# Optimization experiments

Measured on AMD Instinct MI355X. Metric: run time of the kernel, lower is better.

The kernel has to match this reference:

```python
import jax, jax.numpy as jnp
import numpy as np

N = 10000      # nodes
E = 320000     # edges (before self loops)
IN = 128       # in_channels
HID = 128      # hidden_channels
OUT = 64       # out_channels
H = 3          # heads
K = 10         # n_clusters
EDIM = 1       # edge_attr feature dim
NEG_SLOPE = 0.2


def setup_inputs() -> dict:
    key = jax.random.key(0)
    ks = jax.random.split(key, 24)
    x = jax.random.normal(ks[0], (N, IN), jnp.float32)
    src = jax.random.randint(ks[1], (E,), 0, N)
    dst = jax.random.randint(ks[2], (E,), 0, N)
    dst = jnp.where(src == dst, (dst + 1) % N, dst)  # avoid pre-existing self loops
    edge_index = jnp.stack([src, dst]).astype(jnp.int64)
    edge_attr = jax.random.uniform(ks[3], (E, EDIM), dtype=jnp.float32)
    s = 0.1
    inp = {
        'x': x, 'edge_index': edge_index, 'edge_attr': edge_attr,
        # GAT layer 1 params
        'W1': jax.random.normal(ks[4], (IN, H * HID), jnp.float32) * s,
        'att_s1': jax.random.normal(ks[5], (H, HID), jnp.float32) * s,
        'att_d1': jax.random.normal(ks[6], (H, HID), jnp.float32) * s,
        'We1': jax.random.normal(ks[7], (EDIM, H * HID), jnp.float32) * s,
        'att_e1': jax.random.normal(ks[8], (H, HID), jnp.float32) * s,
        'b1': jnp.zeros((H * HID,), jnp.float32),
        # GAT layer 2 params
        'W2': jax.random.normal(ks[9], (H * HID, H * OUT), jnp.float32) * s,
        'att_s2': jax.random.normal(ks[10], (H, OUT), jnp.float32) * s,
        'att_d2': jax.random.normal(ks[11], (H, OUT), jnp.float32) * s,
        'We2': jax.random.normal(ks[12], (EDIM, H * OUT), jnp.float32) * s,
        'att_e2': jax.random.normal(ks[13], (H, OUT), jnp.float32) * s,
        'b2': jnp.zeros((H * OUT,), jnp.float32),
        # cluster head
        'Wp': jax.random.normal(ks[14], (H * OUT, K), jnp.float32) * s,
        'bp': jnp.zeros((K,), jnp.float32),
    }
    return inp


def gat_layer(x, src, dst, eattr, W, att_s, att_d, We, att_e, b, heads, ch):
    n = x.shape[0]
    h = (x @ W).reshape(n, heads, ch)                       # [N,H,C]
    a_s = jnp.einsum('nhc,hc->nh', h, att_s)                # [N,H]
    a_d = jnp.einsum('nhc,hc->nh', h, att_d)
    e = (eattr @ We).reshape(-1, heads, ch)                 # [E,H,C]
    a_e = jnp.einsum('ehc,hc->eh', e, att_e)                # [E,H]
    alpha = jax.nn.leaky_relu(a_s[src] + a_d[dst] + a_e, NEG_SLOPE)
    # segment softmax over destination nodes
    m = jax.ops.segment_max(alpha, dst, num_segments=n)
    ex = jnp.exp(alpha - m[dst])
    denom = jax.ops.segment_sum(ex, dst, num_segments=n)
    coef = ex / (denom[dst] + 1e-16)                        # [E,H]
    msg = h[src] * coef[:, :, None]                         # [E,H,C]
    out = jax.ops.segment_sum(msg, dst, num_segments=n)     # [N,H,C]
    return out.reshape(n, heads * ch) + b


def reference(x, edge_index, edge_attr, W1, att_s1, att_d1, We1, att_e1, b1,
              W2, att_s2, att_d2, We2, att_e2, b2, Wp, bp):
    n = x.shape[0]
    loop = jnp.arange(n, dtype=edge_index.dtype)
    src = jnp.concatenate([edge_index[0], loop])            # add self loops
    dst = jnp.concatenate([edge_index[1], loop])
    ea = jnp.concatenate([edge_attr, jnp.ones((n, edge_attr.shape[1]), edge_attr.dtype)])  # fill_value=1
    h = jnp.nan_to_num(x, nan=0.0)
    h = jax.nn.elu(gat_layer(h, src, dst, ea, W1, att_s1, att_d1, We1, att_e1, b1, H, HID))
    h = gat_layer(h, src, dst, ea, W2, att_s2, att_d2, We2, att_e2, b2, H, OUT)
    z = h / jnp.maximum(jnp.linalg.norm(h, axis=1, keepdims=True), 1e-12)  # F.normalize p=2 dim=1
    A_hat = z @ z.T                                          # [N,N]
    p = jax.nn.softmax(z @ Wp + bp, axis=1)                  # F.softmax picks dim=1 for 2D
    return (A_hat, p, z)
```

## Files before the change

### kernel.cpp

```cpp
#include <hip/hip_runtime.h>
#include <hip/hip_bf16.h>
#include <math.h>

#define NN 10000
#define EE 320000
#define ETOT (EE + NN)
#define INC 128
#define HIDC 128
#define OUTC 64
#define NH 3
#define KCL 10
#define SLOPE 0.2f
#define NPAD 10112

typedef __attribute__((ext_vector_type(8))) short bf16x8;
typedef __attribute__((ext_vector_type(4))) float f32x4;

__device__ __forceinline__ float wave_sum(float v) {
  for (int off = 32; off; off >>= 1) v += __shfl_xor(v, off, 64);
  return v;
}

__device__ __forceinline__ short f2bf(float v) {
  unsigned int u = __float_as_uint(v);
  unsigned int r = (u + 0x7fffu + ((u >> 16) & 1u)) >> 16;
  return (short)r;
}
__device__ __forceinline__ float bf2f(short s) {
  return __uint_as_float(((unsigned int)(unsigned short)s) << 16);
}

__global__ __launch_bounds__(256) void csr_count(const int* __restrict__ dst,
                                                 int* __restrict__ counts,
                                                 int* __restrict__ epos,
                                                 const float* __restrict__ We1,
                                                 const float* __restrict__ ae1,
                                                 const float* __restrict__ We2,
                                                 const float* __restrict__ ae2,
                                                 float* __restrict__ ce) {
  if (blockIdx.x == gridDim.x - 1) {
    int lane = threadIdx.x;
    if (lane < 64) {
      for (int h = 0; h < NH; h++) {
        float p = 0.f;
        for (int c = lane; c < HIDC; c += 64) p += We1[h * HIDC + c] * ae1[h * HIDC + c];
        p = wave_sum(p);
        if (lane == 0) ce[h] = p;
        float q = 0.f;
        for (int c = lane; c < OUTC; c += 64) q += We2[h * OUTC + c] * ae2[h * OUTC + c];
        q = wave_sum(q);
        if (lane == 0) ce[NH + h] = q;
      }
    }
    return;
  }
  int e = blockIdx.x * 256 + threadIdx.x;
  if (e >= ETOT) return;
  int d = (e < EE) ? dst[e] : (e - EE);
  epos[e] = atomicAdd(&counts[d], 1);
}

__global__ __launch_bounds__(1024) void scan_kernel(const int* __restrict__ counts,
                                                    int* __restrict__ offsets) {
  __shared__ int sums[1024];
  const int PT = 10;
  int tid = threadIdx.x;
  int base = tid * PT;
  int loc[PT];
  int run = 0;
#pragma unroll
  for (int j = 0; j < PT; j++) {
    int i = base + j;
    int v = (i < NN) ? counts[i] : 0;
    run += v;
    loc[j] = run;
  }
  sums[tid] = run;
  __syncthreads();
  for (int off = 1; off < 1024; off <<= 1) {
    int t = (tid >= off) ? sums[tid - off] : 0;
    __syncthreads();
    sums[tid] += t;
    __syncthreads();
  }
  int excl = sums[tid] - run;
#pragma unroll
  for (int j = 0; j < PT; j++) {
    int i = base + j;
    if (i < NN) offsets[i + 1] = excl + loc[j];
  }
  if (tid == 0) offsets[0] = 0;
}

__global__ __launch_bounds__(256) void csr_fill(const int* __restrict__ dst,
                                                const int* __restrict__ offsets,
                                                const int* __restrict__ epos,
                                                int* __restrict__ edge_ids) {
  int e = blockIdx.x * 256 + threadIdx.x;
  if (e >= ETOT) return;
  int d = (e < EE) ? dst[e] : (e - EE);
  edge_ids[offsets[d] + epos[e]] = e;
}

template <bool NANFIX>
__global__ __launch_bounds__(256) void gemm_nn_mfma(const float* __restrict__ A,
                                                    const float* __restrict__ B,
                                                    float* __restrict__ C,
                                                    const float* __restrict__ att_s,
                                                    const float* __restrict__ att_d,
                                                    float* __restrict__ as_out,
                                                    float* __restrict__ ad_out,
                                                    int M, int K, int Nc, int ch) {
  __shared__ short Ah[64 * 32], Al[64 * 32];
  __shared__ short Bh[64 * 32], Bl[64 * 32];
  int tid = threadIdx.x;
  int lane = tid & 63, wave = tid >> 6;
  int wm = (wave >> 1) * 32, wn = (wave & 1) * 32;
  int bm = blockIdx.y * 64, bn = blockIdx.x * 64;
  int fr = lane & 15, fk = (lane >> 4) * 8;
  f32x4 acc[2][2] = {};
  int ar = tid >> 2, ac = (tid & 3) * 8;
  int bc = tid & 63, bk0 = tid >> 6;

  for (int k0 = 0; k0 < K; k0 += 32) {
    float av[8];
    if (bm + ar < M) {
      const float* src = A + (size_t)(bm + ar) * K + k0 + ac;
      float4 v0 = *(const float4*)src;
      float4 v1 = *(const float4*)(src + 4);
      av[0] = v0.x; av[1] = v0.y; av[2] = v0.z; av[3] = v0.w;
      av[4] = v1.x; av[5] = v1.y; av[6] = v1.z; av[7] = v1.w;
    } else {
#pragma unroll
      for (int j = 0; j < 8; j++) av[j] = 0.f;
    }
#pragma unroll
    for (int j = 0; j < 8; j++) {
      float v = av[j];
      if (NANFIX) v = (v == v) ? v : 0.f;
      short hs = f2bf(v);
      Ah[ar * 32 + ac + j] = hs;
      Al[ar * 32 + ac + j] = f2bf(v - bf2f(hs));
    }
#pragma unroll
    for (int it = 0; it < 8; it++) {
      int kk = bk0 + it * 4;
      float v = B[(size_t)(k0 + kk) * Nc + bn + bc];
      short hs = f2bf(v);
      Bh[bc * 32 + kk] = hs;
      Bl[bc * 32 + kk] = f2bf(v - bf2f(hs));
    }
    __syncthreads();

    bf16x8 ah[2], al2[2], bh[2], bl2[2];
#pragma unroll
    for (int t = 0; t < 2; t++) {
      ah[t]  = *(const bf16x8*)&Ah[(wm + t * 16 + fr) * 32 + fk];
      al2[t] = *(const bf16x8*)&Al[(wm + t * 16 + fr) * 32 + fk];
      bh[t]  = *(const bf16x8*)&Bh[(wn + t * 16 + fr) * 32 + fk];
      bl2[t] = *(const bf16x8*)&Bl[(wn + t * 16 + fr) * 32 + fk];
    }
#pragma unroll
    for (int i = 0; i < 2; i++)
#pragma unroll
      for (int j = 0; j < 2; j++) {
        acc[i][j] = __builtin_amdgcn_mfma_f32_16x16x32_bf16(ah[i], bh[j], acc[i][j], 0, 0, 0);
        acc[i][j] = __builtin_amdgcn_mfma_f32_16x16x32_bf16(ah[i], bl2[j], acc[i][j], 0, 0, 0);
        acc[i][j] = __builtin_amdgcn_mfma_f32_16x16x32_bf16(al2[i], bh[j], acc[i][j], 0, 0, 0);
      }
    __syncthreads();
  }

  int col0 = lane & 15, rq = (lane >> 4) * 4;
#pragma unroll
  for (int i = 0; i < 2; i++)
#pragma unroll
    for (int v = 0; v < 4; v++) {
      int r = bm + wm + i * 16 + rq + v;
      if (r < M) {
#pragma unroll
        for (int j = 0; j < 2; j++)
          C[(size_t)r * Nc + bn + wn + j * 16 + col0] = acc[i][j][v];
      }
    }

  int head = bn / ch;
  float sax[4], sdx[4];
#pragma unroll
  for (int j = 0; j < 4; j++) {
    int cidx = bn + wn + j * 16 + col0;
    sax[j] = att_s[cidx];
    sdx[j] = att_d[cidx];
  }
#pragma unroll
  for (int i = 0; i < 2; i++)
#pragma unroll
    for (int v = 0; v < 4; v++) {
      float ps = 0.f, pd = 0.f;
#pragma unroll
      for (int j = 0; j < 2; j++) {
        ps += acc[i][j][v] * sax[j];
        pd += acc[i][j][v] * sdx[j];
      }
#pragma unroll
      for (int j = 2; j < 4; j++) {
        ps += acc[i][j & 1][v] * 0.f;
      }
      (void)pd;
      ps = acc[i][0][v] * sax[0] + acc[i][1][v] * sax[1];
      pd = acc[i][0][v] * sdx[0] + acc[i][1][v] * sdx[1];
#pragma unroll
      for (int m = 1; m < 16; m <<= 1) {
        ps += __shfl_xor(ps, m, 64);
        pd += __shfl_xor(pd, m, 64);
      }
      int r = bm + wm + i * 16 + rq + v;
      if ((lane & 15) == 0 && r < M) {
        atomicAdd(&as_out[r * NH + head], ps);
        atomicAdd(&ad_out[r * NH + head], pd);
      }
    }
}

template <int C, bool ELU>
__global__ __launch_bounds__(256) void gat_agg(const float* __restrict__ hfeat,
                                               const float* __restrict__ a_s,
                                               const float* __restrict__ a_d,
                                               const float* __restrict__ ce,
                                               const int* __restrict__ esrc,
                                               const float* __restrict__ ea,
                                               const int* __restrict__ offsets,
                                               const int* __restrict__ edge_ids,
                                               const float* __restrict__ bias,
                                               float* __restrict__ out) {
  const int HC = NH * C;
  int wave = threadIdx.x >> 6, lane = threadIdx.x & 63;
  int n = blockIdx.x * 4 + wave;
  int beg = offsets[n], end = offsets[n + 1];
  float adn0 = a_d[n * NH + 0], adn1 = a_d[n * NH + 1], adn2 = a_d[n * NH + 2];
  float ce0 = ce[0], ce1v = ce[1], ce2 = ce[2];

  float s0 = 0.f, s1 = 0.f, s2 = 0.f;
  float4 a0 = {0.f, 0.f, 0.f, 0.f}, a1 = {0.f, 0.f, 0.f, 0.f};

  for (int base = beg; base < end; base += 64) {
    int i = base + lane;
    int se = 0;
    float e0 = 0.f, e1 = 0.f, e2 = 0.f;
    if (i < end) {
      int e = edge_ids[i];
      float a;
      if (e < EE) { se = esrc[e]; a = ea[e]; } else { se = e - EE; a = 1.f; }
      const float* asr = a_s + NH * se;
      float t0 = asr[0] + adn0 + a * ce0; t0 = t0 > 0.f ? t0 : SLOPE * t0;
      float t1 = asr[1] + adn1 + a * ce1v; t1 = t1 > 0.f ? t1 : SLOPE * t1;
      float t2 = asr[2] + adn2 + a * ce2; t2 = t2 > 0.f ? t2 : SLOPE * t2;
      e0 = __expf(t0); e1 = __expf(t1); e2 = __expf(t2);
      s0 += e0; s1 += e1; s2 += e2;
    }
    int cnt = min(64, end - base);
    for (int t = 0; t < cnt; t++) {
      int s = __shfl(se, t, 64);
      float cc0 = __shfl(e0, t, 64);
      float cc1 = __shfl(e1, t, 64);
      float cc2 = __shfl(e2, t, 64);
      const float4* hr4 = (const float4*)(hfeat + (size_t)s * HC);
      if constexpr (C == 128) {
        float4 v0 = hr4[lane];
        float cA = (lane < 32) ? cc0 : cc1;
        a0.x += v0.x * cA; a0.y += v0.y * cA; a0.z += v0.z * cA; a0.w += v0.w * cA;
        if (lane < 32) {
          float4 v1 = hr4[64 + lane];
          a1.x += v1.x * cc2; a1.y += v1.y * cc2; a1.z += v1.z * cc2; a1.w += v1.w * cc2;
        }
      } else {
        if (lane < 48) {
          float4 v0 = hr4[lane];
          int hd = lane >> 4;
          float cA = (hd == 0) ? cc0 : (hd == 1 ? cc1 : cc2);
          a0.x += v0.x * cA; a0.y += v0.y * cA; a0.z += v0.z * cA; a0.w += v0.w * cA;
        }
      }
    }
  }

  s0 = wave_sum(s0); s1 = wave_sum(s1); s2 = wave_sum(s2);
  float di0 = 1.f / (s0 + 1e-16f), di1 = 1.f / (s1 + 1e-16f), di2 = 1.f / (s2 + 1e-16f);

  if constexpr (C == 128) {
    float dA = (lane < 32) ? di0 : di1;
    float4 b0 = *(const float4*)&bias[4 * lane];
    float x0 = a0.x * dA + b0.x, x1 = a0.y * dA + b0.y;
    float x2 = a0.z * dA + b0.z, x3 = a0.w * dA + b0.w;
    if (ELU) {
      x0 = x0 > 0.f ? x0 : expm1f(x0);
      x1 = x1 > 0.f ? x1 : expm1f(x1);
      x2 = x2 > 0.f ? x2 : expm1f(x2);
      x3 = x3 > 0.f ? x3 : expm1f(x3);
    }
    *(float4*)&out[(size_t)n * HC + 4 * lane] = make_float4(x0, x1, x2, x3);
    if (lane < 32) {
      float4 b1 = *(const float4*)&bias[256 + 4 * lane];
      float y0 = a1.x * di2 + b1.x, y1 = a1.y * di2 + b1.y;
      float y2 = a1.z * di2 + b1.z, y3 = a1.w * di2 + b1.w;
      if (ELU) {
        y0 = y0 > 0.f ? y0 : expm1f(y0);
        y1 = y1 > 0.f ? y1 : expm1f(y1);
        y2 = y2 > 0.f ? y2 : expm1f(y2);
        y3 = y3 > 0.f ? y3 : expm1f(y3);
      }
      *(float4*)&out[(size_t)n * HC + 256 + 4 * lane] = make_float4(y0, y1, y2, y3);
    }
  } else {
    if (lane < 48) {
      int hd = lane >> 4;
      float dA = (hd == 0) ? di0 : (hd == 1 ? di1 : di2);
      float4 b0 = *(const float4*)&bias[4 * lane];
      float x0 = a0.x * dA + b0.x, x1 = a0.y * dA + b0.y;
      float x2 = a0.z * dA + b0.z, x3 = a0.w * dA + b0.w;
      if (ELU) {
        x0 = x0 > 0.f ? x0 : expm1f(x0);
        x1 = x1 > 0.f ? x1 : expm1f(x1);
        x2 = x2 > 0.f ? x2 : expm1f(x2);
        x3 = x3 > 0.f ? x3 : expm1f(x3);
      }
      *(float4*)&out[(size_t)n * HC + 4 * lane] = make_float4(x0, x1, x2, x3);
    }
  }
}

__global__ __launch_bounds__(256) void norm_phead(const float* __restrict__ h2,
                                                  float* __restrict__ z,
                                                  __hip_bfloat16* __restrict__ zb,
                                                  const float* __restrict__ Wp,
                                                  const float* __restrict__ bp,
                                                  float* __restrict__ p) {
  int wave = threadIdx.x >> 6, lane = threadIdx.x & 63;
  int n = blockIdx.x * 4 + wave;
  const float* r = h2 + (size_t)n * 192;
  float v0 = r[lane], v1 = r[lane + 64], v2 = r[lane + 128];
  float s = wave_sum(v0 * v0 + v1 * v1 + v2 * v2);
  float inv = 1.f / fmaxf(sqrtf(s), 1e-12f);
  v0 *= inv; v1 *= inv; v2 *= inv;
  float* zr = z + (size_t)n * 192;
  zr[lane] = v0;
  zr[lane + 64] = v1;
  zr[lane + 128] = v2;
  __hip_bfloat16* zbr = zb + (size_t)n * 192;
  zbr[lane] = __float2bfloat16(v0);
  zbr[lane + 64] = __float2bfloat16(v1);
  zbr[lane + 128] = __float2bfloat16(v2);

  float lg[KCL];
#pragma unroll
  for (int j = 0; j < KCL; j++) {
    float t = v0 * Wp[lane * KCL + j] + v1 * Wp[(lane + 64) * KCL + j] +
              v2 * Wp[(lane + 128) * KCL + j];
    lg[j] = wave_sum(t) + bp[j];
  }
  if (lane == 0) {
    float m = -1e30f;
#pragma unroll
    for (int j = 0; j < KCL; j++) m = fmaxf(m, lg[j]);
    float ex[KCL];
    float sum = 0.f;
#pragma unroll
    for (int j = 0; j < KCL; j++) { ex[j] = expf(lg[j] - m); sum += ex[j]; }
    float invs = 1.f / sum;
#pragma unroll
    for (int j = 0; j < KCL; j++) p[(size_t)n * KCL + j] = ex[j] * invs;
  }
}

__global__ __launch_bounds__(256) void gemm_zzT_mfma(const short* __restrict__ Zb,
                                                     float* __restrict__ C, int N) {
  __shared__ short As[128 * 32];
  __shared__ short Bs[128 * 32];
  int tid = threadIdx.x;
  int lane = tid & 63;
  int wave = tid >> 6;
  int wm = (wave >> 1) * 64, wn = (wave & 1) * 64;
  int bm = blockIdx.y * 128, bn = blockIdx.x * 128;

  f32x4 acc[4][4] = {};

  int lrow = tid >> 2;
  int lcol = (tid & 3) * 8;

  int fr = lane & 15;
  int fk = (lane >> 4) * 8;

  for (int kt = 0; kt < 6; kt++) {
    int k0 = kt * 32;
    const short* ga0 = Zb + (size_t)(bm + lrow) * 192 + k0 + lcol;
    const short* ga1 = Zb + (size_t)(bm + 64 + lrow) * 192 + k0 + lcol;
    const short* gb0 = Zb + (size_t)(bn + lrow) * 192 + k0 + lcol;
    const short* gb1 = Zb + (size_t)(bn + 64 + lrow) * 192 + k0 + lcol;
    __builtin_amdgcn_global_load_lds(
        (const __attribute__((address_space(1))) unsigned int*)ga0,
        (__attribute__((address_space(3))) unsigned int*)&As[lrow * 32 + lcol], 16, 0, 0);
    __builtin_amdgcn_global_load_lds(
        (const __attribute__((address_space(1))) unsigned int*)ga1,
        (__attribute__((address_space(3))) unsigned int*)&As[(64 + lrow) * 32 + lcol], 16, 0, 0);
    __builtin_amdgcn_global_load_lds(
        (const __attribute__((address_space(1))) unsigned int*)gb0,
        (__attribute__((address_space(3))) unsigned int*)&Bs[lrow * 32 + lcol], 16, 0, 0);
    __builtin_amdgcn_global_load_lds(
        (const __attribute__((address_space(1))) unsigned int*)gb1,
        (__attribute__((address_space(3))) unsigned int*)&Bs[(64 + lrow) * 32 + lcol], 16, 0, 0);
    __syncthreads();

    bf16x8 af[4], bfr[4];
#pragma unroll
    for (int t = 0; t < 4; t++) af[t] = *(const bf16x8*)&As[(wm + t * 16 + fr) * 32 + fk];
#pragma unroll
    for (int t = 0; t < 4; t++) bfr[t] = *(const bf16x8*)&Bs[(wn + t * 16 + fr) * 32 + fk];
#pragma unroll
    for (int i = 0; i < 4; i++)
#pragma unroll
      for (int j = 0; j < 4; j++)
        acc[i][j] = __builtin_amdgcn_mfma_f32_16x16x32_bf16(af[i], bfr[j], acc[i][j], 0, 0, 0);
    __syncthreads();
  }

  int col0 = lane & 15;
  int rquad = (lane >> 4) * 4;
#pragma unroll
  for (int i = 0; i < 4; i++) {
#pragma unroll
    for (int v = 0; v < 4; v++) {
      int r = bm + wm + i * 16 + rquad + v;
      if (r >= N) continue;
      size_t ro = (size_t)r * N;
#pragma unroll
      for (int j = 0; j < 4; j++) {
        int c = bn + wn + j * 16 + col0;
        if (c < N) __builtin_nontemporal_store(acc[i][j][v], &C[ro + c]);
      }
    }
  }
}

extern "C" void kernel_launch(void* const* d_in, const int* in_sizes, int n_in,
                              void* d_out, int out_size, void* d_ws, size_t ws_size,
                              hipStream_t stream) {
  const float* x = (const float*)d_in[0];
  const int* edge_index = (const int*)d_in[1];
  const float* edge_attr = (const float*)d_in[2];
  const float* W1 = (const float*)d_in[3];
  const float* att_s1 = (const float*)d_in[4];
  const float* att_d1 = (const float*)d_in[5];
  const float* We1 = (const float*)d_in[6];
  const float* att_e1 = (const float*)d_in[7];
  const float* b1 = (const float*)d_in[8];
  const float* W2 = (const float*)d_in[9];
  const float* att_s2 = (const float*)d_in[10];
  const float* att_d2 = (const float*)d_in[11];
  const float* We2 = (const float*)d_in[12];
  const float* att_e2 = (const float*)d_in[13];
  const float* b2 = (const float*)d_in[14];
  const float* Wp = (const float*)d_in[15];
  const float* bp = (const float*)d_in[16];

  const int* esrc = edge_index;
  const int* edst = edge_index + EE;

  float* A_hat = (float*)d_out;
  float* p_out = A_hat + (size_t)NN * NN;
  float* z_out = p_out + (size_t)NN * KCL;

  char* ws = (char*)d_ws;
  float* h1 = (float*)ws;            ws += sizeof(float) * (size_t)NN * 384;
  float* h1act = (float*)ws;         ws += sizeof(float) * (size_t)NN * 384;
  int* counts = (int*)ws;            ws += sizeof(int) * NN;
  float* as1 = (float*)ws;           ws += sizeof(float) * NN * NH;
  float* ad1 = (float*)ws;           ws += sizeof(float) * NN * NH;
  float* as2 = (float*)ws;           ws += sizeof(float) * NN * NH;
  float* ad2 = (float*)ws;           ws += sizeof(float) * NN * NH;
  float* ce = (float*)ws;            ws += sizeof(float) * 8;
  int* offsets = (int*)ws;           ws += sizeof(int) * (NN + 1);
  int* epos = (int*)ws;              ws += sizeof(int) * ETOT;
  int* edge_ids = (int*)ws;          ws += sizeof(int) * ETOT;
  __hip_bfloat16* zb = (__hip_bfloat16*)ws; ws += sizeof(__hip_bfloat16) * (size_t)NPAD * 192;

  float* h2 = h1;
  float* h2out = h1 + (size_t)NN * 192;

  hipMemsetAsync(counts, 0, sizeof(int) * NN + sizeof(float) * 4 * NN * NH, stream);

  int egrid = (ETOT + 255) / 256;
  csr_count<<<egrid + 1, 256, 0, stream>>>(edst, counts, epos, We1, att_e1, We2, att_e2, ce);
  scan_kernel<<<1, 1024, 0, stream>>>(counts, offsets);
  csr_fill<<<egrid, 256, 0, stream>>>(edst, offsets, epos, edge_ids);

  gemm_nn_mfma<true><<<dim3(384 / 64, (NN + 63) / 64), 256, 0, stream>>>(
      x, W1, h1, att_s1, att_d1, as1, ad1, NN, INC, 384, HIDC);
  gat_agg<HIDC, true><<<NN / 4, 256, 0, stream>>>(h1, as1, ad1, ce, esrc, edge_attr,
                                                  offsets, edge_ids, b1, h1act);

  gemm_nn_mfma<false><<<dim3(192 / 64, (NN + 63) / 64), 256, 0, stream>>>(
      h1act, W2, h2, att_s2, att_d2, as2, ad2, NN, 384, 192, OUTC);
  gat_agg<OUTC, false><<<NN / 4, 256, 0, stream>>>(h2, as2, ad2, ce + NH, esrc, edge_attr,
                                                   offsets, edge_ids, b2, h2out);

  norm_phead<<<NN / 4, 256, 0, stream>>>(h2out, z_out, zb, Wp, bp, p_out);

  gemm_zzT_mfma<<<dim3((NN + 127) / 128, (NN + 127) / 128), 256, 0, stream>>>(
      (const short*)zb, A_hat, NN);
}
```

Before: 686.5 us.

## Pack edge records in CSR, fuse layer-2 aggregation with normalize/head, use 32x32 MFMA

The CSR fill now stores a packed (src, edge_attr) record per sorted edge, so aggregation no longer makes an indirect lookup through edge ids into the source and attribute arrays. The generic aggregation kernel is split into layer-specific versions: layer 1 gets a simpler all-lanes float2 layout, and layer 2 is fused with L2 normalization and the cluster softmax head, which removes one kernel launch and a round-trip of h2out. The zzT GEMM switches from 16x16x32 to 32x32x16 bf16 MFMA tiles, changing fragment loads and the store pattern. In exchange the edge record array doubles in size, and the new store order in the big A_hat write may reduce coalescing.

```diff
diff --git a/kernel.cpp b/kernel.cpp
--- a/kernel.cpp
+++ b/kernel.cpp
@@ -15,6 +15,7 @@
 
 typedef __attribute__((ext_vector_type(8))) short bf16x8;
 typedef __attribute__((ext_vector_type(4))) float f32x4;
+typedef __attribute__((ext_vector_type(16))) float f32x16;
 
 __device__ __forceinline__ float wave_sum(float v) {
   for (int off = 32; off; off >>= 1) v += __shfl_xor(v, off, 64);
@@ -93,13 +94,21 @@
 }
 
 __global__ __launch_bounds__(256) void csr_fill(const int* __restrict__ dst,
+                                                const int* __restrict__ src,
+                                                const float* __restrict__ ea,
                                                 const int* __restrict__ offsets,
                                                 const int* __restrict__ epos,
-                                                int* __restrict__ edge_ids) {
+                                                int2* __restrict__ erec) {
   int e = blockIdx.x * 256 + threadIdx.x;
   if (e >= ETOT) return;
-  int d = (e < EE) ? dst[e] : (e - EE);
-  edge_ids[offsets[d] + epos[e]] = e;
+  int d, s;
+  float a;
+  if (e < EE) {
+    d = dst[e]; s = src[e]; a = ea[e];
+  } else {
+    d = e - EE; s = e - EE; a = 1.f;
+  }
+  erec[offsets[d] + epos[e]] = make_int2(s, __float_as_int(a));
 }
 
 template <bool NANFIX>
@@ -185,30 +194,14 @@
     }
 
   int head = bn / ch;
-  float sax[4], sdx[4];
-#pragma unroll
-  for (int j = 0; j < 4; j++) {
-    int cidx = bn + wn + j * 16 + col0;
-    sax[j] = att_s[cidx];
-    sdx[j] = att_d[cidx];
-  }
+  float sax0 = att_s[bn + wn + col0], sax1 = att_s[bn + wn + 16 + col0];
+  float sdx0 = att_d[bn + wn + col0], sdx1 = att_d[bn + wn + 16 + col0];
 #pragma unroll
   for (int i = 0; i < 2; i++)
 #pragma unroll
     for (int v = 0; v < 4; v++) {
-      float ps = 0.f, pd = 0.f;
-#pragma unroll
-      for (int j = 0; j < 2; j++) {
-        ps += acc[i][j][v] * sax[j];
-        pd += acc[i][j][v] * sdx[j];
-      }
-#pragma unroll
-      for (int j = 2; j < 4; j++) {
-        ps += acc[i][j & 1][v] * 0.f;
-      }
-      (void)pd;
-      ps = acc[i][0][v] * sax[0] + acc[i][1][v] * sax[1];
-      pd = acc[i][0][v] * sdx[0] + acc[i][1][v] * sdx[1];
+      float ps = acc[i][0][v] * sax0 + acc[i][1][v] * sax1;
+      float pd = acc[i][0][v] * sdx0 + acc[i][1][v] * sdx1;
 #pragma unroll
       for (int m = 1; m < 16; m <<= 1) {
         ps += __shfl_xor(ps, m, 64);
@@ -222,18 +215,14 @@
     }
 }
 
-template <int C, bool ELU>
-__global__ __launch_bounds__(256) void gat_agg(const float* __restrict__ hfeat,
-                                               const float* __restrict__ a_s,
-                                               const float* __restrict__ a_d,
-                                               const float* __restrict__ ce,
-                                               const int* __restrict__ esrc,
-                                               const float* __restrict__ ea,
-                                               const int* __restrict__ offsets,
-                                               const int* __restrict__ edge_ids,
-                                               const float* __restrict__ bias,
-                                               float* __restrict__ out) {
-  const int HC = NH * C;
+__global__ __launch_bounds__(256) void gat_agg_l1(const float* __restrict__ hfeat,
+                                                  const float* __restrict__ a_s,
+                                                  const float* __restrict__ a_d,
+                                                  const float* __restrict__ ce,
+                                                  const int* __restrict__ offsets,
+                                                  const int2* __restrict__ erec,
+                                                  const float* __restrict__ bias,
+                                                  float* __restrict__ out) {
   int wave = threadIdx.x >> 6, lane = threadIdx.x & 63;
   int n = blockIdx.x * 4 + wave;
   int beg = offsets[n], end = offsets[n + 1];
@@ -241,16 +230,16 @@
   float ce0 = ce[0], ce1v = ce[1], ce2 = ce[2];
 
   float s0 = 0.f, s1 = 0.f, s2 = 0.f;
-  float4 a0 = {0.f, 0.f, 0.f, 0.f}, a1 = {0.f, 0.f, 0.f, 0.f};
+  float a00 = 0.f, a01 = 0.f, a10 = 0.f, a11 = 0.f, a20 = 0.f, a21 = 0.f;
 
   for (int base = beg; base < end; base += 64) {
     int i = base + lane;
     int se = 0;
     float e0 = 0.f, e1 = 0.f, e2 = 0.f;
     if (i < end) {
-      int e = edge_ids[i];
-      float a;
-      if (e < EE) { se = esrc[e]; a = ea[e]; } else { se = e - EE; a = 1.f; }
+      int2 rec = erec[i];
+      se = rec.x;
+      float a = __int_as_float(rec.y);
       const float* asr = a_s + NH * se;
       float t0 = asr[0] + adn0 + a * ce0; t0 = t0 > 0.f ? t0 : SLOPE * t0;
       float t1 = asr[1] + adn1 + a * ce1v; t1 = t1 > 0.f ? t1 : SLOPE * t1;
@@ -259,77 +248,45 @@
       s0 += e0; s1 += e1; s2 += e2;
     }
     int cnt = min(64, end - base);
+#pragma unroll 2
     for (int t = 0; t < cnt; t++) {
       int s = __shfl(se, t, 64);
-      float cc0 = __shfl(e0, t, 64);
-      float cc1 = __shfl(e1, t, 64);
-      float cc2 = __shfl(e2, t, 64);
-      const float4* hr4 = (const float4*)(hfeat + (size_t)s * HC);
-      if constexpr (C == 128) {
-        float4 v0 = hr4[lane];
-        float cA = (lane < 32) ? cc0 : cc1;
-        a0.x += v0.x * cA; a0.y += v0.y * cA; a0.z += v0.z * cA; a0.w += v0.w * cA;
-        if (lane < 32) {
-          float4 v1 = hr4[64 + lane];
-          a1.x += v1.x * cc2; a1.y += v1.y * cc2; a1.z += v1.z * cc2; a1.w += v1.w * cc2;
-        }
-      } else {
-        if (lane < 48) {
-          float4 v0 = hr4[lane];
-          int hd = lane >> 4;
-          float cA = (hd == 0) ? cc0 : (hd == 1 ? cc1 : cc2);
-          a0.x += v0.x * cA; a0.y += v0.y * cA; a0.z += v0.z * cA; a0.w += v0.w * cA;
-        }
-      }
+      float c0 = __shfl(e0, t, 64);
+      float c1 = __shfl(e1, t, 64);
+      float c2 = __shfl(e2, t, 64);
+      const float2* hr2 = (const float2*)(hfeat + (size_t)s * 384);
+      float2 v0 = hr2[lane], v1 = hr2[lane + 64], v2 = hr2[lane + 128];
+      a00 += v0.x * c0; a01 += v0.y * c0;
+      a10 += v1.x * c1; a11 += v1.y * c1;
+      a20 += v2.x * c2; a21 += v2.y * c2;
     }
   }
 
   s0 = wave_sum(s0); s1 = wave_sum(s1); s2 = wave_sum(s2);
   float di0 = 1.f / (s0 + 1e-16f), di1 = 1.f / (s1 + 1e-16f), di2 = 1.f / (s2 + 1e-16f);
 
-  if constexpr (C == 128) {
-    float dA = (lane < 32) ? di0 : di1;
-    float4 b0 = *(const float4*)&bias[4 * lane];
-    float x0 = a0.x * dA + b0.x, x1 = a0.y * dA + b0.y;
-    float x2 = a0.z * dA + b0.z, x3 = a0.w * dA + b0.w;
-    if (ELU) {
-      x0 = x0 > 0.f ? x0 : expm1f(x0);
-      x1 = x1 > 0.f ? x1 : expm1f(x1);
-      x2 = x2 > 0.f ? x2 : expm1f(x2);
-      x3 = x3 > 0.f ? x3 : expm1f(x3);
-    }
-    *(float4*)&out[(size_t)n * HC + 4 * lane] = make_float4(x0, x1, x2, x3);
-    if (lane < 32) {
-      float4 b1 = *(const float4*)&bias[256 + 4 * lane];
-      float y0 = a1.x * di2 + b1.x, y1 = a1.y * di2 + b1.y;
-      float y2 = a1.z * di2 + b1.z, y3 = a1.w * di2 + b1.w;
-      if (ELU) {
-        y0 = y0 > 0.f ? y0 : expm1f(y0);
-        y1 = y1 > 0.f ? y1 : expm1f(y1);
-        y2 = y2 > 0.f ? y2 : expm1f(y2);
-        y3 = y3 > 0.f ? y3 : expm1f(y3);
-      }
-      *(float4*)&out[(size_t)n * HC + 256 + 4 * lane] = make_float4(y0, y1, y2, y3);
-    }
-  } else {
-    if (lane < 48) {
-      int hd = lane >> 4;
-      float dA = (hd == 0) ? di0 : (hd == 1 ? di1 : di2);
-      float4 b0 = *(const float4*)&bias[4 * lane];
-      float x0 = a0.x * dA + b0.x, x1 = a0.y * dA + b0.y;
-      float x2 = a0.z * dA + b0.z, x3 = a0.w * dA + b0.w;
-      if (ELU) {
-        x0 = x0 > 0.f ? x0 : expm1f(x0);
-        x1 = x1 > 0.f ? x1 : expm1f(x1);
-        x2 = x2 > 0.f ? x2 : expm1f(x2);
-        x3 = x3 > 0.f ? x3 : expm1f(x3);
-      }
-      *(float4*)&out[(size_t)n * HC + 4 * lane] = make_float4(x0, x1, x2, x3);
-    }
-  }
-}
-
-__global__ __launch_bounds__(256) void norm_phead(const float* __restrict__ h2,
+  float2 b0 = *(const float2*)&bias[2 * lane];
+  float2 b1 = *(const float2*)&bias[128 + 2 * lane];
+  float2 b2 = *(const float2*)&bias[256 + 2 * lane];
+  float x0 = a00 * di0 + b0.x, x1 = a01 * di0 + b0.y;
+  float y0 = a10 * di1 + b1.x, y1 = a11 * di1 + b1.y;
+  float z0 = a20 * di2 + b2.x, z1 = a21 * di2 + b2.y;
+  x0 = x0 > 0.f ? x0 : expm1f(x0); x1 = x1 > 0.f ? x1 : expm1f(x1);
+  y0 = y0 > 0.f ? y0 : expm1f(y0); y1 = y1 > 0.f ? y1 : expm1f(y1);
+  z0 = z0 > 0.f ? z0 : expm1f(z0); z1 = z1 > 0.f ? z1 : expm1f(z1);
+  float* orow = out + (size_t)n * 384;
+  *(float2*)&orow[2 * lane] = make_float2(x0, x1);
+  *(float2*)&orow[128 + 2 * lane] = make_float2(y0, y1);
+  *(float2*)&orow[256 + 2 * lane] = make_float2(z0, z1);
+}
+
+__global__ __launch_bounds__(256) void gat_agg_l2(const float* __restrict__ hfeat,
+                                                  const float* __restrict__ a_s,
+                                                  const float* __restrict__ a_d,
+                                                  const float* __restrict__ ce,
+                                                  const int* __restrict__ offsets,
+                                                  const int2* __restrict__ erec,
+                                                  const float* __restrict__ bias,
                                                   float* __restrict__ z,
                                                   __hip_bfloat16* __restrict__ zb,
                                                   const float* __restrict__ Wp,
@@ -337,25 +294,63 @@
                                                   float* __restrict__ p) {
   int wave = threadIdx.x >> 6, lane = threadIdx.x & 63;
   int n = blockIdx.x * 4 + wave;
-  const float* r = h2 + (size_t)n * 192;
-  float v0 = r[lane], v1 = r[lane + 64], v2 = r[lane + 128];
-  float s = wave_sum(v0 * v0 + v1 * v1 + v2 * v2);
-  float inv = 1.f / fmaxf(sqrtf(s), 1e-12f);
-  v0 *= inv; v1 *= inv; v2 *= inv;
+  int beg = offsets[n], end = offsets[n + 1];
+  float adn0 = a_d[n * NH + 0], adn1 = a_d[n * NH + 1], adn2 = a_d[n * NH + 2];
+  float ce0 = ce[0], ce1v = ce[1], ce2 = ce[2];
+
+  float s0 = 0.f, s1 = 0.f, s2 = 0.f;
+  float a0 = 0.f, a1 = 0.f, a2 = 0.f;
+
+  for (int base = beg; base < end; base += 64) {
+    int i = base + lane;
+    int se = 0;
+    float e0 = 0.f, e1 = 0.f, e2 = 0.f;
+    if (i < end) {
+      int2 rec = erec[i];
+      se = rec.x;
+      float a = __int_as_float(rec.y);
+      const float* asr = a_s + NH * se;
+      float t0 = asr[0] + adn0 + a * ce0; t0 = t0 > 0.f ? t0 : SLOPE * t0;
+      float t1 = asr[1] + adn1 + a * ce1v; t1 = t1 > 0.f ? t1 : SLOPE * t1;
+      float t2 = asr[2] + adn2 + a * ce2; t2 = t2 > 0.f ? t2 : SLOPE * t2;
+      e0 = __expf(t0); e1 = __expf(t1); e2 = __expf(t2);
+      s0 += e0; s1 += e1; s2 += e2;
+    }
+    int cnt = min(64, end - base);
+#pragma unroll 2
+    for (int t = 0; t < cnt; t++) {
+      int s = __shfl(se, t, 64);
+      float c0 = __shfl(e0, t, 64);
+      float c1 = __shfl(e1, t, 64);
+      float c2 = __shfl(e2, t, 64);
+      const float* hr = hfeat + (size_t)s * 192;
+      a0 += hr[lane] * c0;
+      a1 += hr[lane + 64] * c1;
+      a2 += hr[lane + 128] * c2;
+    }
+  }
+
+  s0 = wave_sum(s0); s1 = wave_sum(s1); s2 = wave_sum(s2);
+  float x0 = a0 / (s0 + 1e-16f) + bias[lane];
+  float x1 = a1 / (s1 + 1e-16f) + bias[lane + 64];
+  float x2 = a2 / (s2 + 1e-16f) + bias[lane + 128];
+
+  float sq = wave_sum(x0 * x0 + x1 * x1 + x2 * x2);
+  float inv = 1.f / fmaxf(sqrtf(sq), 1e-12f);
+  x0 *= inv; x1 *= inv; x2 *= inv;
+
   float* zr = z + (size_t)n * 192;
-  zr[lane] = v0;
-  zr[lane + 64] = v1;
-  zr[lane + 128] = v2;
+  zr[lane] = x0; zr[lane + 64] = x1; zr[lane + 128] = x2;
   __hip_bfloat16* zbr = zb + (size_t)n * 192;
-  zbr[lane] = __float2bfloat16(v0);
-  zbr[lane + 64] = __float2bfloat16(v1);
-  zbr[lane + 128] = __float2bfloat16(v2);
+  zbr[lane] = __float2bfloat16(x0);
+  zbr[lane + 64] = __float2bfloat16(x1);
+  zbr[lane + 128] = __float2bfloat16(x2);
 
   float lg[KCL];
 #pragma unroll
   for (int j = 0; j < KCL; j++) {
-    float t = v0 * Wp[lane * KCL + j] + v1 * Wp[(lane + 64) * KCL + j] +
-              v2 * Wp[(lane + 128) * KCL + j];
+    float t = x0 * Wp[lane * KCL + j] + x1 * Wp[(lane + 64) * KCL + j] +
+              x2 * Wp[(lane + 128) * KCL + j];
     lg[j] = wave_sum(t) + bp[j];
   }
   if (lane == 0) {
@@ -382,13 +377,13 @@
   int wm = (wave >> 1) * 64, wn = (wave & 1) * 64;
   int bm = blockIdx.y * 128, bn = blockIdx.x * 128;
 
-  f32x4 acc[4][4] = {};
+  f32x16 acc[2][2] = {};
 
   int lrow = tid >> 2;
   int lcol = (tid & 3) * 8;
 
-  int fr = lane & 15;
-  int fk = (lane >> 4) * 8;
+  int fr = lane & 31;
+  int fk = (lane >> 5) * 8;
 
   for (int kt = 0; kt < 6; kt++) {
     int k0 = kt * 32;
@@ -410,32 +405,37 @@
         (__attribute__((address_space(3))) unsigned int*)&Bs[(64 + lrow) * 32 + lcol], 16, 0, 0);
     __syncthreads();
 
-    bf16x8 af[4], bfr[4];
-#pragma unroll
-    for (int t = 0; t < 4; t++) af[t] = *(const bf16x8*)&As[(wm + t * 16 + fr) * 32 + fk];
-#pragma unroll
-    for (int t = 0; t < 4; t++) bfr[t] = *(const bf16x8*)&Bs[(wn + t * 16 + fr) * 32 + fk];
-#pragma unroll
-    for (int i = 0; i < 4; i++)
-#pragma unroll
-      for (int j = 0; j < 4; j++)
-        acc[i][j] = __builtin_amdgcn_mfma_f32_16x16x32_bf16(af[i], bfr[j], acc[i][j], 0, 0, 0);
+    bf16x8 af[2][2], bfr[2][2];
+#pragma unroll
+    for (int t = 0; t < 2; t++)
+#pragma unroll
+      for (int ks = 0; ks < 2; ks++) {
+        af[t][ks] = *(const bf16x8*)&As[(wm + t * 32 + fr) * 32 + ks * 16 + fk];
+        bfr[t][ks] = *(const bf16x8*)&Bs[(wn + t * 32 + fr) * 32 + ks * 16 + fk];
+      }
+#pragma unroll
+    for (int i = 0; i < 2; i++)
+#pragma unroll
+      for (int j = 0; j < 2; j++)
+#pragma unroll
+        for (int ks = 0; ks < 2; ks++)
+          acc[i][j] = __builtin_amdgcn_mfma_f32_32x32x16_bf16(af[i][ks], bfr[j][ks],
+                                                              acc[i][j], 0, 0, 0);
     __syncthreads();
   }
 
-  int col0 = lane & 15;
-  int rquad = (lane >> 4) * 4;
-#pragma unroll
-  for (int i = 0; i < 4; i++) {
-#pragma unroll
-    for (int v = 0; v < 4; v++) {
-      int r = bm + wm + i * 16 + rquad + v;
-      if (r >= N) continue;
-      size_t ro = (size_t)r * N;
-#pragma unroll
-      for (int j = 0; j < 4; j++) {
-        int c = bn + wn + j * 16 + col0;
-        if (c < N) __builtin_nontemporal_store(acc[i][j][v], &C[ro + c]);
+  int col0 = lane & 31;
+  int rbase = 4 * (lane >> 5);
+#pragma unroll
+  for (int i = 0; i < 2; i++) {
+#pragma unroll
+    for (int j = 0; j < 2; j++) {
+      int c = bn + wn + j * 32 + col0;
+      if (c >= N) continue;
+#pragma unroll
+      for (int r = 0; r < 16; r++) {
+        int row = bm + wm + i * 32 + (r & 3) + 8 * (r >> 2) + rbase;
+        if (row < N) __builtin_nontemporal_store(acc[i][j][r], &C[(size_t)row * N + c]);
       }
     }
   }
@@ -478,32 +478,28 @@
   float* as2 = (float*)ws;           ws += sizeof(float) * NN * NH;
   float* ad2 = (float*)ws;           ws += sizeof(float) * NN * NH;
   float* ce = (float*)ws;            ws += sizeof(float) * 8;
-  int* offsets = (int*)ws;           ws += sizeof(int) * (NN + 1);
+  int* offsets = (int*)ws;           ws += sizeof(int) * (NN + 4);
   int* epos = (int*)ws;              ws += sizeof(int) * ETOT;
-  int* edge_ids = (int*)ws;          ws += sizeof(int) * ETOT;
+  int2* erec = (int2*)ws;            ws += sizeof(int2) * ETOT;
   __hip_bfloat16* zb = (__hip_bfloat16*)ws; ws += sizeof(__hip_bfloat16) * (size_t)NPAD * 192;
 
   float* h2 = h1;
-  float* h2out = h1 + (size_t)NN * 192;
 
   hipMemsetAsync(counts, 0, sizeof(int) * NN + sizeof(float) * 4 * NN * NH, stream);
 
   int egrid = (ETOT + 255) / 256;
   csr_count<<<egrid + 1, 256, 0, stream>>>(edst, counts, epos, We1, att_e1, We2, att_e2, ce);
   scan_kernel<<<1, 1024, 0, stream>>>(counts, offsets);
-  csr_fill<<<egrid, 256, 0, stream>>>(edst, offsets, epos, edge_ids);
+  csr_fill<<<egrid, 256, 0, stream>>>(edst, esrc, edge_attr, offsets, epos, erec);
 
   gemm_nn_mfma<true><<<dim3(384 / 64, (NN + 63) / 64), 256, 0, stream>>>(
       x, W1, h1, att_s1, att_d1, as1, ad1, NN, INC, 384, HIDC);
-  gat_agg<HIDC, true><<<NN / 4, 256, 0, stream>>>(h1, as1, ad1, ce, esrc, edge_attr,
-                                                  offsets, edge_ids, b1, h1act);
+  gat_agg_l1<<<NN / 4, 256, 0, stream>>>(h1, as1, ad1, ce, offsets, erec, b1, h1act);
 
   gemm_nn_mfma<false><<<dim3(192 / 64, (NN + 63) / 64), 256, 0, stream>>>(
       h1act, W2, h2, att_s2, att_d2, as2, ad2, NN, 384, 192, OUTC);
-  gat_agg<OUTC, false><<<NN / 4, 256, 0, stream>>>(h2, as2, ad2, ce + NH, esrc, edge_attr,
-                                                   offsets, edge_ids, b2, h2out);
-
-  norm_phead<<<NN / 4, 256, 0, stream>>>(h2out, z_out, zb, Wp, bp, p_out);
+  gat_agg_l2<<<NN / 4, 256, 0, stream>>>(h2, as2, ad2, ce + NH, offsets, erec, b2,
+                                         z_out, zb, Wp, bp, p_out);
 
   gemm_zzT_mfma<<<dim3((NN + 127) / 128, (NN + 127) / 128), 256, 0, stream>>>(
       (const short*)zb, A_hat, NN);
```

Result: faster. 653.5 us (-4.8%).
